# Kernel tuning notes

Measured on AMD Instinct MI355X. Metric: run time of the kernel, lower is better.

Reference implementation:

```python
import jax, jax.numpy as jnp
import numpy as np


def _trilinear_sample(src, iz, iy, ix):
    """grid_sample 3D, mode='bilinear' (trilinear), padding_mode='zeros', on unnormalized voxel coords.
    src: [B,C,D,H,W]; iz,iy,ix: [B,D,H,W] float voxel coords (iz indexes D, iy H, ix W)."""
    B, C, D, H, W = src.shape
    z0 = jnp.floor(iz); y0 = jnp.floor(iy); x0 = jnp.floor(ix)
    tz = iz - z0; ty = iy - y0; tx = ix - x0
    z0i = z0.astype(jnp.int32); y0i = y0.astype(jnp.int32); x0i = x0.astype(jnp.int32)
    src_flat = src.reshape(B, C, D * H * W)

    def corner(dz, dy, dx):
        zc = z0i + dz; yc = y0i + dy; xc = x0i + dx
        valid = (zc >= 0) & (zc < D) & (yc >= 0) & (yc < H) & (xc >= 0) & (xc < W)
        zcc = jnp.clip(zc, 0, D - 1); ycc = jnp.clip(yc, 0, H - 1); xcc = jnp.clip(xc, 0, W - 1)
        lin = (zcc * H + ycc) * W + xcc                      # [B,D,H,W] flat spatial index
        vals = jax.vmap(lambda v, i: v[:, i.ravel()])(src_flat, lin)  # [B,C,D*H*W]
        vals = vals.reshape(B, C, D, H, W)
        wz = tz if dz else (1.0 - tz)
        wy = ty if dy else (1.0 - ty)
        wx = tx if dx else (1.0 - tx)
        w = (wz * wy * wx) * valid.astype(src.dtype)         # zeros padding
        return vals * w[:, None]

    out = jnp.zeros_like(src)
    for dz in (0, 1):
        for dy in (0, 1):
            for dx in (0, 1):
                out = out + corner(dz, dy, dx)
    return out


def reference(src, flow):
    B, _, D, H, W = flow.shape
    dt = flow.dtype
    # identity grid, channels ordered (z,y,x) i.e. (D,H,W), matching torch.meshgrid indexing='ij'
    gz, gy, gx = jnp.meshgrid(jnp.arange(D, dtype=dt), jnp.arange(H, dtype=dt),
                              jnp.arange(W, dtype=dt), indexing='ij')
    grid = jnp.stack([gz, gy, gx])[None]                     # [1,3,D,H,W]
    coords = grid + flow                                      # absolute voxel coords
    denom = jnp.array([D - 1, H - 1, W - 1], dtype=dt).reshape(1, 3, 1, 1, 1)
    norm = 2.0 * (coords / denom - 0.5)                       # normalized to [-1,1]
    # grid_sample expects last-dim order (x,y,z); align_corners=True unnormalization:
    ix = (norm[:, 2] + 1.0) * (W - 1) * 0.5
    iy = (norm[:, 1] + 1.0) * (H - 1) * 0.5
    iz = (norm[:, 0] + 1.0) * (D - 1) * 0.5
    return _trilinear_sample(src, iz, iy, ix)


def setup_inputs() -> dict:
    key = jax.random.key(0)
    k1, k2 = jax.random.split(key)
    B, C, D, H, W = 2, 2, 128, 160, 128
    src = jax.random.normal(k1, (B, C, D, H, W), dtype=jnp.float32)
    flow = jax.random.normal(k2, (B, 3, D, H, W), dtype=jnp.float32)
    return {"src": src, "flow": flow}
```

## Files before the change

kernel.cpp:

```cpp
#include <hip/hip_runtime.h>
#include <hip/hip_bf16.h>


#define B_ 2
#define C_ 2
#define D_ 128
#define H_ 160
#define W_ 128
constexpr int S_ = D_ * H_ * W_;

#define ZT 4
#define YT 8
#define XT 32
#define RZ 3
#define RY 3
#define RX 4
#define CZ (ZT + 2 * RZ)
#define CY (YT + 2 * RY)
#define CX (XT + 2 * RX)
#define NTHREADS 256
#define VPT ((ZT * YT * XT) / NTHREADS)
#define NCHUNK (CZ * CY * (CX / 4))

__device__ __forceinline__ float pair_val(const float* p, bool hi0, bool lo1,
                                          float wx0, float wx1) {
    const float v0 = hi0 ? p[1] : p[0];
    const float v1 = lo1 ? p[0] : p[1];
    return wx0 * v0 + wx1 * v1;
}

__global__ __launch_bounds__(NTHREADS, 4) void warp3d_tile(
    const float* __restrict__ src,
    const float* __restrict__ flow,
    float* __restrict__ out)
{
    __shared__ float tile[CZ * CY * CX];

    const int tid = threadIdx.x;
    const int xb = blockIdx.x * XT;
    const int yb = blockIdx.y * YT;
    const int bz = blockIdx.z;
    const int zb = (bz & 31) * ZT;
    const int b  = (bz >> 6);
    const int ch = (bz >> 5) & 1;

    const int zlo = max(0, zb - RZ), zhi = min(D_, zb + ZT + RZ);
    const int ylo = max(0, yb - RY), yhi = min(H_, yb + YT + RY);
    const int xlo = max(0, xb - RX), xhi = min(W_, xb + XT + RX);

    const float* fb = flow + (long long)b * 3 * S_;
    const float* sc = src + ((long long)b * C_ + ch) * S_;
    float* oc       = out + ((long long)b * C_ + ch) * S_;

#pragma unroll
    for (int j = 0; j < 6; ++j) {
        const int lin = j * NTHREADS + tid;
        if (lin < NCHUNK) {
            const int row = lin / 10;
            const int c   = lin - row * 10;
            const int rz = row / CY, ry = row - rz * CY;
            const int gz = zb - RZ + rz;
            const int gy = yb - RY + ry;
            const int gx = xb - RX + c * 4;
            if ((unsigned)gz < (unsigned)D_ && (unsigned)gy < (unsigned)H_ &&
                (unsigned)gx <= (unsigned)(W_ - 4)) {
                const float4 v = *(const float4*)(sc + ((gz * H_ + gy) << 7) + gx);
                *(float4*)&tile[row * CX + c * 4] = v;
            }
        }
    }
    __syncthreads();

#pragma unroll
    for (int it = 0; it < VPT; ++it) {
        const int vox = it * NTHREADS + tid;
        const int lx = vox & 31, ly = (vox >> 5) & 7, lz = vox >> 8;
        const int x = xb + lx, y = yb + ly, z = zb + lz;
        const int s = ((z * H_ + y) << 7) + x;

        const float fz = fb[s], fy = fb[S_ + s], fx = fb[2 * S_ + s];
        const float iz = (float)z + fz;
        const float iy = (float)y + fy;
        const float ix = (float)x + fx;

        const float zf = floorf(iz), yf = floorf(iy), xf = floorf(ix);
        const float tz = iz - zf, ty = iy - yf, tx = ix - xf;
        const int z0 = (int)zf, y0 = (int)yf, x0 = (int)xf;

        const int zc0 = min(max(z0, 0), D_ - 1), zc1 = min(max(z0 + 1, 0), D_ - 1);
        const int yc0 = min(max(y0, 0), H_ - 1), yc1 = min(max(y0 + 1, 0), H_ - 1);
        const int xp  = min(max(x0, 0), W_ - 2);

        const float wz0 = ((unsigned)z0       < (unsigned)D_) ? (1.f - tz) : 0.f;
        const float wz1 = ((unsigned)(z0 + 1) < (unsigned)D_) ? tz         : 0.f;
        const float wy0 = ((unsigned)y0       < (unsigned)H_) ? (1.f - ty) : 0.f;
        const float wy1 = ((unsigned)(y0 + 1) < (unsigned)H_) ? ty         : 0.f;
        const float wx0 = ((unsigned)x0       < (unsigned)W_) ? (1.f - tx) : 0.f;
        const float wx1 = ((unsigned)(x0 + 1) < (unsigned)W_) ? tx         : 0.f;
        const bool hi0 = x0 > xp;
        const bool lo1 = x0 < xp;

        const bool fast = (zc0 >= zlo) & (zc1 < zhi) &
                          (yc0 >= ylo) & (yc1 < yhi) &
                          (xp >= xlo) & (xp + 1 < xhi);

        float acc;
        if (fast) {
            const int izl0 = zc0 - (zb - RZ), izl1 = zc1 - (zb - RZ);
            const int iyl0 = yc0 - (yb - RY), iyl1 = yc1 - (yb - RY);
            const int ixl  = xp - (xb - RX);
            const float* t00 = &tile[(izl0 * CY + iyl0) * CX + ixl];
            const float* t01 = &tile[(izl0 * CY + iyl1) * CX + ixl];
            const float* t10 = &tile[(izl1 * CY + iyl0) * CX + ixl];
            const float* t11 = &tile[(izl1 * CY + iyl1) * CX + ixl];
            const float p00 = pair_val(t00, hi0, lo1, wx0, wx1);
            const float p01 = pair_val(t01, hi0, lo1, wx0, wx1);
            const float p10 = pair_val(t10, hi0, lo1, wx0, wx1);
            const float p11 = pair_val(t11, hi0, lo1, wx0, wx1);
            acc = wz0 * (wy0 * p00 + wy1 * p01) + wz1 * (wy0 * p10 + wy1 * p11);
        } else {
            const float* g00 = sc + ((zc0 * H_ + yc0) << 7) + xp;
            const float* g01 = sc + ((zc0 * H_ + yc1) << 7) + xp;
            const float* g10 = sc + ((zc1 * H_ + yc0) << 7) + xp;
            const float* g11 = sc + ((zc1 * H_ + yc1) << 7) + xp;
            const float p00 = pair_val(g00, hi0, lo1, wx0, wx1);
            const float p01 = pair_val(g01, hi0, lo1, wx0, wx1);
            const float p10 = pair_val(g10, hi0, lo1, wx0, wx1);
            const float p11 = pair_val(g11, hi0, lo1, wx0, wx1);
            acc = wz0 * (wy0 * p00 + wy1 * p01) + wz1 * (wy0 * p10 + wy1 * p11);
        }
        oc[s] = acc;
    }
}

extern "C" void kernel_launch(void* const* d_in, const int* in_sizes, int n_in,
                              void* d_out, int out_size, void* d_ws, size_t ws_size,
                              hipStream_t stream) {
    const float* src  = (const float*)d_in[0];
    const float* flow = (const float*)d_in[1];
    float* out = (float*)d_out;

    dim3 grid(W_ / XT, H_ / YT, (D_ / ZT) * C_ * B_);
    warp3d_tile<<<grid, NTHREADS, 0, stream>>>(src, flow, out);
}
```

Measured before the change: 164.4 us.

## Process both source channels per block with channel-interleaved LDS tile

```diff
diff --git a/kernel.cpp b/kernel.cpp
--- a/kernel.cpp
+++ b/kernel.cpp
@@ -1,5 +1,4 @@
 #include <hip/hip_runtime.h>
-#include <hip/hip_bf16.h>
 
 
 #define B_ 2
@@ -18,9 +17,10 @@
 #define CZ (ZT + 2 * RZ)
 #define CY (YT + 2 * RY)
 #define CX (XT + 2 * RX)
-#define NTHREADS 256
-#define VPT ((ZT * YT * XT) / NTHREADS)
-#define NCHUNK (CZ * CY * (CX / 4))
+#define NTHREADS 512
+#define NPAIR (ZT * YT * XT)
+#define PPT (NPAIR / NTHREADS)
+#define NCHUNK (CZ * CY * (CX / 2))
 
 __device__ __forceinline__ float pair_val(const float* p, bool hi0, bool lo1,
                                           float wx0, float wx1) {
@@ -29,50 +29,63 @@
     return wx0 * v0 + wx1 * v1;
 }
 
-__global__ __launch_bounds__(NTHREADS, 4) void warp3d_tile(
+__device__ __forceinline__ float2 lds_pair2(const float* t, int o,
+                                            bool hi0, bool lo1,
+                                            float wx0, float wx1) {
+    const float2 a = *(const float2*)&t[o];
+    const float2 b = *(const float2*)&t[o + 2];
+    const float v00 = hi0 ? b.x : a.x;
+    const float v01 = lo1 ? a.x : b.x;
+    const float v10 = hi0 ? b.y : a.y;
+    const float v11 = lo1 ? a.y : b.y;
+    return make_float2(wx0 * v00 + wx1 * v01, wx0 * v10 + wx1 * v11);
+}
+
+__global__ __launch_bounds__(NTHREADS, 6) void warp3d_tile(
     const float* __restrict__ src,
     const float* __restrict__ flow,
     float* __restrict__ out)
 {
-    __shared__ float tile[CZ * CY * CX];
+    __shared__ float tile[CZ * CY * CX * 2];
 
     const int tid = threadIdx.x;
     const int xb = blockIdx.x * XT;
     const int yb = blockIdx.y * YT;
     const int bz = blockIdx.z;
     const int zb = (bz & 31) * ZT;
-    const int b  = (bz >> 6);
-    const int ch = (bz >> 5) & 1;
+    const int b  = bz >> 5;
 
     const int zlo = max(0, zb - RZ), zhi = min(D_, zb + ZT + RZ);
     const int ylo = max(0, yb - RY), yhi = min(H_, yb + YT + RY);
     const int xlo = max(0, xb - RX), xhi = min(W_, xb + XT + RX);
 
     const float* fb = flow + (long long)b * 3 * S_;
-    const float* sc = src + ((long long)b * C_ + ch) * S_;
-    float* oc       = out + ((long long)b * C_ + ch) * S_;
+    const float* s0 = src + (long long)b * C_ * S_;
+    float* o0       = out + (long long)b * C_ * S_;
 
 #pragma unroll
     for (int j = 0; j < 6; ++j) {
         const int lin = j * NTHREADS + tid;
         if (lin < NCHUNK) {
-            const int row = lin / 10;
-            const int c   = lin - row * 10;
+            const int row = lin / 20;
+            const int c   = lin - row * 20;
             const int rz = row / CY, ry = row - rz * CY;
             const int gz = zb - RZ + rz;
             const int gy = yb - RY + ry;
-            const int gx = xb - RX + c * 4;
+            const int gx = xb - RX + c * 2;
             if ((unsigned)gz < (unsigned)D_ && (unsigned)gy < (unsigned)H_ &&
-                (unsigned)gx <= (unsigned)(W_ - 4)) {
-                const float4 v = *(const float4*)(sc + ((gz * H_ + gy) << 7) + gx);
-                *(float4*)&tile[row * CX + c * 4] = v;
+                (unsigned)gx <= (unsigned)(W_ - 2)) {
+                const int off = ((gz * H_ + gy) << 7) + gx;
+                const float2 va = *(const float2*)(s0 + off);
+                const float2 vb = *(const float2*)(s0 + S_ + off);
+                *(float4*)&tile[lin * 4] = make_float4(va.x, vb.x, va.y, vb.y);
             }
         }
     }
     __syncthreads();
 
 #pragma unroll
-    for (int it = 0; it < VPT; ++it) {
+    for (int it = 0; it < PPT; ++it) {
         const int vox = it * NTHREADS + tid;
         const int lx = vox & 31, ly = (vox >> 5) & 7, lz = vox >> 8;
         const int x = xb + lx, y = yb + ly, z = zb + lz;
@@ -104,32 +117,39 @@
                           (yc0 >= ylo) & (yc1 < yhi) &
                           (xp >= xlo) & (xp + 1 < xhi);
 
-        float acc;
+        float acc0, acc1;
         if (fast) {
             const int izl0 = zc0 - (zb - RZ), izl1 = zc1 - (zb - RZ);
             const int iyl0 = yc0 - (yb - RY), iyl1 = yc1 - (yb - RY);
             const int ixl  = xp - (xb - RX);
-            const float* t00 = &tile[(izl0 * CY + iyl0) * CX + ixl];
-            const float* t01 = &tile[(izl0 * CY + iyl1) * CX + ixl];
-            const float* t10 = &tile[(izl1 * CY + iyl0) * CX + ixl];
-            const float* t11 = &tile[(izl1 * CY + iyl1) * CX + ixl];
-            const float p00 = pair_val(t00, hi0, lo1, wx0, wx1);
-            const float p01 = pair_val(t01, hi0, lo1, wx0, wx1);
-            const float p10 = pair_val(t10, hi0, lo1, wx0, wx1);
-            const float p11 = pair_val(t11, hi0, lo1, wx0, wx1);
-            acc = wz0 * (wy0 * p00 + wy1 * p01) + wz1 * (wy0 * p10 + wy1 * p11);
+            const int o00 = ((izl0 * CY + iyl0) * CX + ixl) * 2;
+            const int o01 = ((izl0 * CY + iyl1) * CX + ixl) * 2;
+            const int o10 = ((izl1 * CY + iyl0) * CX + ixl) * 2;
+            const int o11 = ((izl1 * CY + iyl1) * CX + ixl) * 2;
+            const float2 p00 = lds_pair2(tile, o00, hi0, lo1, wx0, wx1);
+            const float2 p01 = lds_pair2(tile, o01, hi0, lo1, wx0, wx1);
+            const float2 p10 = lds_pair2(tile, o10, hi0, lo1, wx0, wx1);
+            const float2 p11 = lds_pair2(tile, o11, hi0, lo1, wx0, wx1);
+            acc0 = wz0 * (wy0 * p00.x + wy1 * p01.x) + wz1 * (wy0 * p10.x + wy1 * p11.x);
+            acc1 = wz0 * (wy0 * p00.y + wy1 * p01.y) + wz1 * (wy0 * p10.y + wy1 * p11.y);
         } else {
-            const float* g00 = sc + ((zc0 * H_ + yc0) << 7) + xp;
-            const float* g01 = sc + ((zc0 * H_ + yc1) << 7) + xp;
-            const float* g10 = sc + ((zc1 * H_ + yc0) << 7) + xp;
-            const float* g11 = sc + ((zc1 * H_ + yc1) << 7) + xp;
-            const float p00 = pair_val(g00, hi0, lo1, wx0, wx1);
-            const float p01 = pair_val(g01, hi0, lo1, wx0, wx1);
-            const float p10 = pair_val(g10, hi0, lo1, wx0, wx1);
-            const float p11 = pair_val(g11, hi0, lo1, wx0, wx1);
-            acc = wz0 * (wy0 * p00 + wy1 * p01) + wz1 * (wy0 * p10 + wy1 * p11);
+            const int l00 = ((zc0 * H_ + yc0) << 7) + xp;
+            const int l01 = ((zc0 * H_ + yc1) << 7) + xp;
+            const int l10 = ((zc1 * H_ + yc0) << 7) + xp;
+            const int l11 = ((zc1 * H_ + yc1) << 7) + xp;
+            const float q00 = pair_val(s0 + l00, hi0, lo1, wx0, wx1);
+            const float q01 = pair_val(s0 + l01, hi0, lo1, wx0, wx1);
+            const float q10 = pair_val(s0 + l10, hi0, lo1, wx0, wx1);
+            const float q11 = pair_val(s0 + l11, hi0, lo1, wx0, wx1);
+            const float r00 = pair_val(s0 + S_ + l00, hi0, lo1, wx0, wx1);
+            const float r01 = pair_val(s0 + S_ + l01, hi0, lo1, wx0, wx1);
+            const float r10 = pair_val(s0 + S_ + l10, hi0, lo1, wx0, wx1);
+            const float r11 = pair_val(s0 + S_ + l11, hi0, lo1, wx0, wx1);
+            acc0 = wz0 * (wy0 * q00 + wy1 * q01) + wz1 * (wy0 * q10 + wy1 * q11);
+            acc1 = wz0 * (wy0 * r00 + wy1 * r01) + wz1 * (wy0 * r10 + wy1 * r11);
         }
-        oc[s] = acc;
+        o0[s]      = acc0;
+        o0[S_ + s] = acc1;
     }
 }
 
@@ -140,6 +160,6 @@
     const float* flow = (const float*)d_in[1];
     float* out = (float*)d_out;
 
-    dim3 grid(W_ / XT, H_ / YT, (D_ / ZT) * C_ * B_);
+    dim3 grid(W_ / XT, H_ / YT, (D_ / ZT) * B_);
     warp3d_tile<<<grid, NTHREADS, 0, stream>>>(src, flow, out);
 }
```

Result: no change. 163.1 us (-0.8%).
